# Optimization experiments

Measured on AMD Instinct MI355X. Metric: run time of the kernel, lower is better.

## Reference

```python
import jax, jax.numpy as jnp
import numpy as np

N_NODES = 50000
N_EDGES = 1600000
LORA_R = 8


def gcn_conv(h, W, b, src, dst, n):
    # PyG GCNConv: linear transform, add self-loops, symmetric normalization,
    # scatter-add aggregation at target nodes, then bias.
    h = h @ W  # [N, out]
    ones = jnp.ones(src.shape[0], dtype=h.dtype)
    deg = jax.ops.segment_sum(ones, dst, num_segments=n) + 1.0  # +1 for self-loop
    dis = jax.lax.rsqrt(deg)  # deg >= 1 always
    norm = dis[src] * dis[dst]  # [E]
    agg = jax.ops.segment_sum(norm[:, None] * h[src], dst, num_segments=n)
    agg = agg + (dis * dis)[:, None] * h  # self-loop contribution
    return agg + b


def lora(h, A, B):
    # LoRALinear: b(a(x)) * (1/r); replaces input (not additive)
    return (h @ A) @ B * (1.0 / LORA_R)


def setup_inputs() -> dict:
    key = jax.random.key(0)
    ks = jax.random.split(key, 12)
    inp = {}
    inp['x'] = jax.random.normal(ks[0], (N_NODES, 128), dtype=jnp.float32)
    inp['edge_index'] = jax.random.randint(ks[1], (2, N_EDGES), 0, N_NODES, dtype=jnp.int64 if jax.config.jax_enable_x64 else jnp.int32)
    inp['domain_idx'] = jax.random.randint(ks[2], (N_NODES,), 0, 3, dtype=jnp.int32)
    inp['emb_table'] = jax.random.normal(ks[3], (3, 4096), dtype=jnp.float32)
    s1 = 1.0 / np.sqrt(4224.0)
    inp['W1'] = jax.random.normal(ks[4], (4224, 32), dtype=jnp.float32) * s1
    inp['b1'] = jnp.zeros((32,), dtype=jnp.float32)
    inp['A1'] = jax.random.normal(ks[5], (32, LORA_R), dtype=jnp.float32) * (1.0 / np.sqrt(32.0))
    inp['B1'] = jax.random.normal(ks[6], (LORA_R, 32), dtype=jnp.float32) * (1.0 / np.sqrt(LORA_R))
    inp['W2'] = jax.random.normal(ks[7], (32, 5), dtype=jnp.float32) * (1.0 / np.sqrt(32.0))
    inp['b2'] = jnp.zeros((5,), dtype=jnp.float32)
    inp['A2'] = jax.random.normal(ks[8], (5, LORA_R), dtype=jnp.float32) * (1.0 / np.sqrt(5.0))
    inp['B2'] = jax.random.normal(ks[9], (LORA_R, 5), dtype=jnp.float32) * (1.0 / np.sqrt(LORA_R))
    return inp


def reference(x, edge_index, domain_idx, emb_table, W1, b1, A1, B1, W2, b2, A2, B2):
    n = x.shape[0]
    src, dst = edge_index[0], edge_index[1]
    embedded = emb_table[domain_idx]  # [N, 4096]
    h = jnp.concatenate([embedded, x], axis=1)  # [N, 4224]
    h = gcn_conv(h, W1, b1, src, dst, n)
    h = lora(h, A1, B1)
    h = jax.nn.relu(h)
    h = gcn_conv(h, W2, b2, src, dst, n)
    h = lora(h, A2, B2)
    return jax.nn.log_softmax(h, axis=1)
```

## Files before the change

kernel.cpp:

```cpp
#include <hip/hip_runtime.h>
#include <hip/hip_bf16.h>
#include <hip/hip_fp16.h>


#define XDIM 128
#define EMBDIM 4096
#define TB 4096
#define BSH 6
#define BN 64
#define ECAP2 2560

__global__ void __launch_bounds__(256) kA(
    const int* __restrict__ src, const int* __restrict__ dst,
    unsigned int* __restrict__ tedges, unsigned int* __restrict__ toffcnt,
    int e, int ntiles,
    const float* __restrict__ emb, const float* __restrict__ W1,
    float* __restrict__ emb_part,
    const float* __restrict__ A1, const float* __restrict__ A2,
    const float* __restrict__ B2, const float* __restrict__ b1,
    float* __restrict__ M2, float* __restrict__ b1A1,
    const float* __restrict__ x, float* __restrict__ g, int n) {
    __shared__ __align__(16) char smem[24576];
    int t = threadIdx.x, bx = blockIdx.x;
    if (bx < ntiles) {
        unsigned int* staged = (unsigned int*)smem;
        int* loff = (int*)(smem + 16384);
        int* rctr = (int*)(smem + 20480);
        int base = bx * TB;
        int len = min(TB, e - base);
        for (int i = t; i < 1024; i += 256) { loff[i] = 0; rctr[i] = 0; }
        __syncthreads();
        for (int i = t; i < len; i += 256) atomicAdd(&loff[dst[base + i] >> BSH], 1);
        __syncthreads();
        if (t < 64) {
            int ch = t * 16;
            int v[16]; int s0 = 0;
            #pragma unroll
            for (int k = 0; k < 16; ++k) { v[k] = loff[ch + k]; s0 += v[k]; }
            int pre = s0;
            #pragma unroll
            for (int d2 = 1; d2 < 64; d2 <<= 1) {
                int up = __shfl_up(pre, d2);
                if (t >= d2) pre += up;
            }
            int excl = pre - s0;
            unsigned int* ocp = toffcnt + (size_t)bx * 1024 + ch;
            #pragma unroll
            for (int k = 0; k < 16; ++k) {
                loff[ch + k] = excl;
                ocp[k] = ((unsigned int)excl << 16) | (unsigned int)v[k];
                excl += v[k];
            }
        }
        __syncthreads();
        for (int i = t; i < len; i += 256) {
            int s = src[base + i], d = dst[base + i];
            int b = d >> BSH;
            int r = atomicAdd(&rctr[b], 1);
            staged[loff[b] + r] = ((unsigned int)d << 16) | (unsigned int)s;
        }
        __syncthreads();
        uint4* tw = (uint4*)(tedges + (size_t)bx * TB);
        const uint4* sr = (const uint4*)staged;
        int lw = (len + 3) >> 2;
        for (int i = t; i < lw; i += 256) tw[i] = sr[i];
    } else if (bx < ntiles + 96) {
        float* red = (float*)smem;
        int bx2 = bx - ntiles;
        int dm = bx2 >> 5, seg = bx2 & 31;
        const float* er = emb + dm * EMBDIM + seg * 128;
        const float* wr = W1 + (size_t)(seg * 128) * 32;
        int j = t & 31, kk = t >> 5;
        float acc = 0.f;
        for (int k2 = kk; k2 < 128; k2 += 8) acc += er[k2] * wr[k2 * 32 + j];
        red[kk * 32 + j] = acc;
        __syncthreads();
        if (t < 32) {
            float s = 0.f;
            #pragma unroll
            for (int r = 0; r < 8; ++r) s += red[r * 32 + t];
            emb_part[bx2 * 32 + t] = s;
        }
        if (bx2 == 0) {
            if (t < 25) {
                int c = t / 5, cp = t % 5;
                float s = 0.f;
                #pragma unroll
                for (int r = 0; r < 8; ++r) s += A2[c * 8 + r] * B2[r * 5 + cp];
                M2[c * 5 + cp] = s * 0.125f;
            }
            if (t >= 32 && t < 40) {
                int j2 = t - 32;
                float s = 0.f;
                #pragma unroll
                for (int k = 0; k < 32; ++k) s += b1[k] * A1[k * 8 + j2];
                b1A1[j2] = s;
            }
        }
    } else {
        __half* xsh = (__half*)smem;
        float* sWA  = (float*)(smem + 16384);
        float* sA1  = (float*)(smem + 20480);
        int gb = bx - ntiles - 96;
        int row0 = gb * 64;
        sA1[t] = A1[t];
        for (int i = t; i < 2048; i += 256) {
            int row = i >> 5, c4 = i & 31;
            int gi = row0 + row;
            float4 v = (gi < n) ? ((const float4*)x)[(size_t)gi * 32 + c4]
                                : make_float4(0.f, 0.f, 0.f, 0.f);
            __half2 h01 = __floats2half2_rn(v.x, v.y);
            __half2 h23 = __floats2half2_rn(v.z, v.w);
            uint2 pk;
            pk.x = *(unsigned int*)&h01;
            pk.y = *(unsigned int*)&h23;
            *(uint2*)(xsh + row * 128 + c4 * 4) = pk;
        }
        __syncthreads();
        for (int idx = t; idx < 1024; idx += 256) {
            int k = idx >> 3, j = idx & 7;
            const float* wr = W1 + (size_t)(EMBDIM + k) * 32;
            float s = 0.f;
            #pragma unroll 8
            for (int c = 0; c < 32; ++c) s += wr[c] * sA1[c * 8 + j];
            sWA[idx] = s;
        }
        __syncthreads();
        int row = t >> 3, j = t & 7;
        const __half2* xr1 = (const __half2*)(xsh + row * 128);
        const __half2* xr2 = (const __half2*)(xsh + (row + 32) * 128);
        float acc1 = 0.f, acc2 = 0.f;
        #pragma unroll 8
        for (int k2 = 0; k2 < 64; ++k2) {
            float2 fa = __half22float2(xr1[k2]);
            float2 fb = __half22float2(xr2[k2]);
            float w0 = sWA[(2 * k2) * 8 + j];
            float w1 = sWA[(2 * k2 + 1) * 8 + j];
            acc1 += fa.x * w0 + fa.y * w1;
            acc2 += fb.x * w0 + fb.y * w1;
        }
        int gi1 = row0 + row, gi2 = row0 + row + 32;
        if (gi1 < n) g[(size_t)gi1 * 8 + j] = acc1;
        if (gi2 < n) g[(size_t)gi2 * 8 + j] = acc2;
    }
}

__global__ void __launch_bounds__(256) kB(
    const unsigned int* __restrict__ tedges, const unsigned int* __restrict__ toffcnt,
    int ntiles,
    const float* __restrict__ emb_part, const float* __restrict__ A1,
    const int* __restrict__ dom, const float* __restrict__ g,
    int* __restrict__ deg, __half* __restrict__ p1h,
    unsigned short* __restrict__ nsrc, unsigned int* __restrict__ bm, int n) {
    __shared__ int hist[64], eoff[64], rctr[64], sdom[64];
    __shared__ int mcur;
    __shared__ float sA1[256], sproj[96], sembA1[24];
    __shared__ __align__(16) unsigned int ebuf[ECAP2];
    __shared__ __align__(16) unsigned short esrc[ECAP2];
    int t = threadIdx.x, b = blockIdx.x;
    int row0 = b << BSH;
    if (t == 0) mcur = 0;
    if (t < 64) {
        hist[t] = 0; rctr[t] = 0;
        int gi = row0 + t;
        sdom[t] = (gi < n) ? dom[gi] : 0;
    }
    sA1[t] = A1[t];
    if (t < 96) {
        int dm = t >> 5, c = t & 31;
        float s = 0.f;
        #pragma unroll
        for (int seg = 0; seg < 32; ++seg) s += emb_part[(dm * 32 + seg) * 32 + c];
        sproj[dm * 32 + c] = s;
    }
    __syncthreads();
    for (int tl = t; tl < ntiles; tl += 256) {
        unsigned int oc = toffcnt[(size_t)tl * 1024 + b];
        int len = (int)(oc & 0xffffu);
        if (len > 0) {
            int dstb = atomicAdd(&mcur, len);
            const unsigned int* rp = tedges + (size_t)tl * TB + (oc >> 16);
            for (int j = 0; j < len; ++j) {
                int p = dstb + j;
                if (p < ECAP2) ebuf[p] = rp[j];
            }
        }
    }
    __syncthreads();
    int m = mcur;
    if (m > ECAP2) m = ECAP2;
    if (t == 0) bm[b] = (unsigned int)m;
    for (int i = t; i < m; i += 256) atomicAdd(&hist[(ebuf[i] >> 16) & (BN - 1)], 1);
    __syncthreads();
    if (t < 64) {
        int v = hist[t];
        int pre = v;
        #pragma unroll
        for (int d2 = 1; d2 < 64; d2 <<= 1) {
            int up = __shfl_up(pre, d2);
            if (t >= d2) pre += up;
        }
        eoff[t] = pre - v;
        int gi = row0 + t;
        if (gi < n) deg[gi] = v;
    } else if (t < 88) {
        int dm = (t - 64) >> 3, j = (t - 64) & 7;
        float s = 0.f;
        #pragma unroll 8
        for (int c = 0; c < 32; ++c) s += sproj[dm * 32 + c] * sA1[c * 8 + j];
        sembA1[dm * 8 + j] = s;
    }
    __syncthreads();
    for (int i = t; i < m; i += 256) {
        unsigned int u = ebuf[i];
        int dl = (int)(u >> 16) & (BN - 1);
        int r = atomicAdd(&rctr[dl], 1);
        esrc[eoff[dl] + r] = (unsigned short)(u & 0xffffu);
    }
    for (int i = t; i < 512; i += 256) {
        int row = i >> 3, j = i & 7;
        int gi = row0 + row;
        if (gi < n) {
            float dd = rsqrtf((float)(hist[row] + 1));
            float v = g[(size_t)gi * 8 + j] + sembA1[sdom[row] * 8 + j];
            p1h[(size_t)gi * 8 + j] = __float2half_rn(dd * v);
        }
    }
    __syncthreads();
    {
        uint4* npw = (uint4*)(nsrc + (size_t)b * ECAP2);
        const uint4* ew = (const uint4*)esrc;
        int mw = (m + 7) >> 3;
        for (int i = t; i < mw; i += 256) npw[i] = ew[i];
    }
}

__global__ void __launch_bounds__(256) k_bagg1(
    const __half* __restrict__ p1h, const unsigned short* __restrict__ nsrc,
    const unsigned int* __restrict__ bm, const int* __restrict__ deg,
    const float* __restrict__ b1A1, const float* __restrict__ B1,
    const float* __restrict__ W2, __half* __restrict__ qh, int n) {
    __shared__ __align__(16) unsigned short esrc[ECAP2];
    __shared__ int eoff[BN], sdeg[BN];
    __shared__ float pacc[3][BN][8];
    __shared__ float sB1[256], sW2[160], sb[8];
    int t = threadIdx.x, b = blockIdx.x;
    int node0 = b << BSH;
    sB1[t] = B1[t];
    if (t < 160) sW2[t] = W2[t];
    if (t < 8) sb[t] = b1A1[t];
    if (t < 64) {
        int node = node0 + t;
        int v = (node < n) ? deg[node] : 0;
        sdeg[t] = v;
        int pre = v;
        #pragma unroll
        for (int d2 = 1; d2 < 64; d2 <<= 1) {
            int up = __shfl_up(pre, d2);
            if (t >= d2) pre += up;
        }
        eoff[t] = pre - v;
    }
    __syncthreads();
    int m = (int)bm[b];
    if (m > ECAP2) m = ECAP2;
    {
        const uint4* npw = (const uint4*)(nsrc + (size_t)b * ECAP2);
        uint4* ew = (uint4*)esrc;
        int mw = (m + 7) >> 3;
        for (int i = t; i < mw; i += 256) ew[i] = npw[i];
    }
    __syncthreads();
    int nodeL = t & (BN - 1), tsub = t >> BSH;
    int base0 = eoff[nodeL], c = sdeg[nodeL];
    float a[8] = {0.f, 0.f, 0.f, 0.f, 0.f, 0.f, 0.f, 0.f};
    float a2[8] = {0.f, 0.f, 0.f, 0.f, 0.f, 0.f, 0.f, 0.f};
    int k = tsub;
    for (; k + 4 < c; k += 8) {
        int s1 = esrc[base0 + k], s2 = esrc[base0 + k + 4];
        uint4 u = *(const uint4*)(p1h + (size_t)s1 * 8);
        uint4 v = *(const uint4*)(p1h + (size_t)s2 * 8);
        float2 f;
        f = __half22float2(*(__half2*)&u.x); a[0] += f.x; a[1] += f.y;
        f = __half22float2(*(__half2*)&u.y); a[2] += f.x; a[3] += f.y;
        f = __half22float2(*(__half2*)&u.z); a[4] += f.x; a[5] += f.y;
        f = __half22float2(*(__half2*)&u.w); a[6] += f.x; a[7] += f.y;
        f = __half22float2(*(__half2*)&v.x); a2[0] += f.x; a2[1] += f.y;
        f = __half22float2(*(__half2*)&v.y); a2[2] += f.x; a2[3] += f.y;
        f = __half22float2(*(__half2*)&v.z); a2[4] += f.x; a2[5] += f.y;
        f = __half22float2(*(__half2*)&v.w); a2[6] += f.x; a2[7] += f.y;
    }
    for (; k < c; k += 4) {
        int s1 = esrc[base0 + k];
        uint4 u = *(const uint4*)(p1h + (size_t)s1 * 8);
        float2 f;
        f = __half22float2(*(__half2*)&u.x); a[0] += f.x; a[1] += f.y;
        f = __half22float2(*(__half2*)&u.y); a[2] += f.x; a[3] += f.y;
        f = __half22float2(*(__half2*)&u.z); a[4] += f.x; a[5] += f.y;
        f = __half22float2(*(__half2*)&u.w); a[6] += f.x; a[7] += f.y;
    }
    #pragma unroll
    for (int j = 0; j < 8; ++j) a[j] += a2[j];
    if (tsub > 0) {
        #pragma unroll
        for (int j = 0; j < 8; ++j) pacc[tsub - 1][nodeL][j] = a[j];
    }
    __syncthreads();
    if (t < BN) {
        int node = node0 + t;
        if (node < n) {
            float dd = rsqrtf((float)(sdeg[t] + 1));
            uint4 u = *(const uint4*)(p1h + (size_t)node * 8);
            float2 f;
            float af[8];
            f = __half22float2(*(__half2*)&u.x); af[0] = a[0] + f.x; af[1] = a[1] + f.y;
            f = __half22float2(*(__half2*)&u.y); af[2] = a[2] + f.x; af[3] = a[3] + f.y;
            f = __half22float2(*(__half2*)&u.z); af[4] = a[4] + f.x; af[5] = a[5] + f.y;
            f = __half22float2(*(__half2*)&u.w); af[6] = a[6] + f.x; af[7] = a[7] + f.y;
            #pragma unroll
            for (int ps = 0; ps < 3; ++ps) {
                #pragma unroll
                for (int j = 0; j < 8; ++j) af[j] += pacc[ps][t][j];
            }
            #pragma unroll
            for (int j = 0; j < 8; ++j) af[j] = dd * af[j] + sb[j];
            float qv[5] = {0.f, 0.f, 0.f, 0.f, 0.f};
            #pragma unroll
            for (int c2 = 0; c2 < 32; ++c2) {
                float tv = 0.f;
                #pragma unroll
                for (int j = 0; j < 8; ++j) tv += af[j] * sB1[j * 32 + c2];
                float st = fmaxf(tv * 0.125f, 0.f);
                #pragma unroll
                for (int o = 0; o < 5; ++o) qv[o] += st * sW2[c2 * 5 + o];
            }
            #pragma unroll
            for (int o = 0; o < 5; ++o) qh[(size_t)node * 8 + o] = __float2half_rn(dd * qv[o]);
        }
    }
}

__global__ void __launch_bounds__(256) k_bagg2(
    const __half* __restrict__ qh, const unsigned short* __restrict__ nsrc,
    const unsigned int* __restrict__ bm, const int* __restrict__ deg,
    const float* __restrict__ b2, const float* __restrict__ M2,
    float* __restrict__ out, int n) {
    __shared__ __align__(16) unsigned short esrc[ECAP2];
    __shared__ int eoff[BN], sdeg[BN];
    __shared__ float pacc[3][BN][5];
    __shared__ float sM2[25], sb2[5];
    int t = threadIdx.x, b = blockIdx.x;
    int node0 = b << BSH;
    if (t < 25) sM2[t] = M2[t];
    if (t < 5) sb2[t] = b2[t];
    if (t < 64) {
        int node = node0 + t;
        int v = (node < n) ? deg[node] : 0;
        sdeg[t] = v;
        int pre = v;
        #pragma unroll
        for (int d2 = 1; d2 < 64; d2 <<= 1) {
            int up = __shfl_up(pre, d2);
            if (t >= d2) pre += up;
        }
        eoff[t] = pre - v;
    }
    __syncthreads();
    int m = (int)bm[b];
    if (m > ECAP2) m = ECAP2;
    {
        const uint4* npw = (const uint4*)(nsrc + (size_t)b * ECAP2);
        uint4* ew = (uint4*)esrc;
        int mw = (m + 7) >> 3;
        for (int i = t; i < mw; i += 256) ew[i] = npw[i];
    }
    __syncthreads();
    int nodeL = t & (BN - 1), tsub = t >> BSH;
    int base0 = eoff[nodeL], c = sdeg[nodeL];
    float a[5] = {0.f, 0.f, 0.f, 0.f, 0.f};
    float a2[5] = {0.f, 0.f, 0.f, 0.f, 0.f};
    int k = tsub;
    for (; k + 4 < c; k += 8) {
        int s1 = esrc[base0 + k], s2 = esrc[base0 + k + 4];
        uint4 u = *(const uint4*)(qh + (size_t)s1 * 8);
        uint4 v = *(const uint4*)(qh + (size_t)s2 * 8);
        float2 f;
        f = __half22float2(*(__half2*)&u.x); a[0] += f.x; a[1] += f.y;
        f = __half22float2(*(__half2*)&u.y); a[2] += f.x; a[3] += f.y;
        f = __half22float2(*(__half2*)&u.z); a[4] += f.x;
        f = __half22float2(*(__half2*)&v.x); a2[0] += f.x; a2[1] += f.y;
        f = __half22float2(*(__half2*)&v.y); a2[2] += f.x; a2[3] += f.y;
        f = __half22float2(*(__half2*)&v.z); a2[4] += f.x;
    }
    for (; k < c; k += 4) {
        int s1 = esrc[base0 + k];
        uint4 u = *(const uint4*)(qh + (size_t)s1 * 8);
        float2 f;
        f = __half22float2(*(__half2*)&u.x); a[0] += f.x; a[1] += f.y;
        f = __half22float2(*(__half2*)&u.y); a[2] += f.x; a[3] += f.y;
        f = __half22float2(*(__half2*)&u.z); a[4] += f.x;
    }
    #pragma unroll
    for (int j = 0; j < 5; ++j) a[j] += a2[j];
    if (tsub > 0) {
        #pragma unroll
        for (int j = 0; j < 5; ++j) pacc[tsub - 1][nodeL][j] = a[j];
    }
    __syncthreads();
    if (t < BN) {
        int node = node0 + t;
        if (node < n) {
            float dd = rsqrtf((float)(sdeg[t] + 1));
            uint4 u = *(const uint4*)(qh + (size_t)node * 8);
            float2 f;
            float av[5];
            f = __half22float2(*(__half2*)&u.x); av[0] = a[0] + f.x; av[1] = a[1] + f.y;
            f = __half22float2(*(__half2*)&u.y); av[2] = a[2] + f.x; av[3] = a[3] + f.y;
            f = __half22float2(*(__half2*)&u.z); av[4] = a[4] + f.x;
            #pragma unroll
            for (int ps = 0; ps < 3; ++ps) {
                #pragma unroll
                for (int j = 0; j < 5; ++j) av[j] += pacc[ps][t][j];
            }
            #pragma unroll
            for (int j = 0; j < 5; ++j) av[j] = dd * av[j] + sb2[j];
            float z[5];
            #pragma unroll
            for (int cp = 0; cp < 5; ++cp) {
                float s = 0.f;
                #pragma unroll
                for (int c2 = 0; c2 < 5; ++c2) s += av[c2] * sM2[c2 * 5 + cp];
                z[cp] = s;
            }
            float mx = z[0];
            #pragma unroll
            for (int c2 = 1; c2 < 5; ++c2) mx = fmaxf(mx, z[c2]);
            float ssum = 0.f;
            #pragma unroll
            for (int c2 = 0; c2 < 5; ++c2) ssum += __expf(z[c2] - mx);
            float ls = __logf(ssum);
            #pragma unroll
            for (int c2 = 0; c2 < 5; ++c2) out[node * 5 + c2] = z[c2] - mx - ls;
        }
    }
}

extern "C" void kernel_launch(void* const* d_in, const int* in_sizes, int n_in,
                              void* d_out, int out_size, void* d_ws, size_t ws_size,
                              hipStream_t stream) {
    const float* x   = (const float*)d_in[0];
    const int*   ei  = (const int*)d_in[1];
    const int*   dom = (const int*)d_in[2];
    const float* emb = (const float*)d_in[3];
    const float* W1  = (const float*)d_in[4];
    const float* b1  = (const float*)d_in[5];
    const float* A1  = (const float*)d_in[6];
    const float* B1  = (const float*)d_in[7];
    const float* W2  = (const float*)d_in[8];
    const float* b2  = (const float*)d_in[9];
    const float* A2  = (const float*)d_in[10];
    const float* B2  = (const float*)d_in[11];
    float* out = (float*)d_out;

    int n = in_sizes[2];
    int e = in_sizes[1] / 2;
    const int* src = ei;
    const int* dst = ei + e;

    int ntiles = (e + TB - 1) / TB;
    int nbuck  = (n + BN - 1) >> BSH;
    int ngb    = (n + 63) / 64;

    char* base = (char*)d_ws;
    size_t o = 0;
    auto carve = [&](size_t bytes) {
        void* p = base + o;
        o = (o + bytes + 15) & ~(size_t)15;
        return p;
    };
    float* emb_part = (float*)carve(96 * 32 * sizeof(float));
    float* M2       = (float*)carve(32 * sizeof(float));
    float* b1A1     = (float*)carve(8 * sizeof(float));
    unsigned int* bm = (unsigned int*)carve(1024 * sizeof(int));
    int*   deg      = (int*)carve((size_t)n * sizeof(int));
    float* g        = (float*)carve((size_t)n * 8 * sizeof(float));
    __half* p1h     = (__half*)carve((size_t)n * 8 * sizeof(__half));
    __half* qh      = (__half*)carve((size_t)n * 8 * sizeof(__half));
    unsigned int* tedges  = (unsigned int*)carve((size_t)ntiles * TB * sizeof(unsigned int));
    unsigned int* toffcnt = (unsigned int*)carve((size_t)ntiles * 1024 * sizeof(unsigned int));
    unsigned short* nsrc  = (unsigned short*)carve((size_t)nbuck * ECAP2 * sizeof(unsigned short));
    (void)ws_size; (void)n_in; (void)out_size;

    kA<<<ntiles + 96 + ngb, 256, 0, stream>>>(
        src, dst, tedges, toffcnt, e, ntiles,
        emb, W1, emb_part, A1, A2, B2, b1, M2, b1A1, x, g, n);
    kB<<<nbuck, 256, 0, stream>>>(tedges, toffcnt, ntiles, emb_part, A1, dom, g,
                                  deg, p1h, nsrc, bm, n);
    k_bagg1<<<nbuck, 256, 0, stream>>>(p1h, nsrc, bm, deg, b1A1, B1, W2, qh, n);
    k_bagg2<<<nbuck, 256, 0, stream>>>(qh, nsrc, bm, deg, b2, M2, out, n);
}
```

Baseline: 158.0 us.

## Cache edge loads in registers and prefix-scan tile offsets for cooperative gather

```diff
diff --git a/kernel.cpp b/kernel.cpp
--- a/kernel.cpp
+++ b/kernel.cpp
@@ -9,6 +9,7 @@
 #define BSH 6
 #define BN 64
 #define ECAP2 2560
+#define MAXT 512
 
 __global__ void __launch_bounds__(256) kA(
     const int* __restrict__ src, const int* __restrict__ dst,
@@ -30,7 +31,20 @@
         int len = min(TB, e - base);
         for (int i = t; i < 1024; i += 256) { loff[i] = 0; rctr[i] = 0; }
         __syncthreads();
-        for (int i = t; i < len; i += 256) atomicAdd(&loff[dst[base + i] >> BSH], 1);
+        int sreg[16], dreg[16];
+        #pragma unroll
+        for (int k = 0; k < 16; ++k) {
+            int i = t + k * 256;
+            if (i < len) {
+                sreg[k] = src[base + i];
+                dreg[k] = dst[base + i];
+            }
+        }
+        #pragma unroll
+        for (int k = 0; k < 16; ++k) {
+            int i = t + k * 256;
+            if (i < len) atomicAdd(&loff[dreg[k] >> BSH], 1);
+        }
         __syncthreads();
         if (t < 64) {
             int ch = t * 16;
@@ -53,11 +67,14 @@
             }
         }
         __syncthreads();
-        for (int i = t; i < len; i += 256) {
-            int s = src[base + i], d = dst[base + i];
-            int b = d >> BSH;
-            int r = atomicAdd(&rctr[b], 1);
-            staged[loff[b] + r] = ((unsigned int)d << 16) | (unsigned int)s;
+        #pragma unroll
+        for (int k = 0; k < 16; ++k) {
+            int i = t + k * 256;
+            if (i < len) {
+                int b = dreg[k] >> BSH;
+                int r = atomicAdd(&rctr[b], 1);
+                staged[loff[b] + r] = ((unsigned int)dreg[k] << 16) | (unsigned int)sreg[k];
+            }
         }
         __syncthreads();
         uint4* tw = (uint4*)(tedges + (size_t)bx * TB);
@@ -153,13 +170,13 @@
     int* __restrict__ deg, __half* __restrict__ p1h,
     unsigned short* __restrict__ nsrc, unsigned int* __restrict__ bm, int n) {
     __shared__ int hist[64], eoff[64], rctr[64], sdom[64];
-    __shared__ int mcur;
+    __shared__ int mtot;
+    __shared__ unsigned short rbase[MAXT], soff[MAXT], slen[MAXT];
     __shared__ float sA1[256], sproj[96], sembA1[24];
     __shared__ __align__(16) unsigned int ebuf[ECAP2];
     __shared__ __align__(16) unsigned short esrc[ECAP2];
     int t = threadIdx.x, b = blockIdx.x;
     int row0 = b << BSH;
-    if (t == 0) mcur = 0;
     if (t < 64) {
         hist[t] = 0; rctr[t] = 0;
         int gi = row0 + t;
@@ -173,23 +190,47 @@
         for (int seg = 0; seg < 32; ++seg) s += emb_part[(dm * 32 + seg) * 32 + c];
         sproj[dm * 32 + c] = s;
     }
-    __syncthreads();
-    for (int tl = t; tl < ntiles; tl += 256) {
-        unsigned int oc = toffcnt[(size_t)tl * 1024 + b];
-        int len = (int)(oc & 0xffffu);
-        if (len > 0) {
-            int dstb = atomicAdd(&mcur, len);
-            const unsigned int* rp = tedges + (size_t)tl * TB + (oc >> 16);
-            for (int j = 0; j < len; ++j) {
-                int p = dstb + j;
-                if (p < ECAP2) ebuf[p] = rp[j];
-            }
-        }
-    }
-    __syncthreads();
-    int m = mcur;
+    if (t < 64) {
+        int carry = 0;
+        int nch = (ntiles + 63) >> 6;
+        for (int c = 0; c < nch; ++c) {
+            int idx = (c << 6) + t;
+            unsigned int oc = (idx < ntiles) ? toffcnt[(size_t)idx * 1024 + b] : 0u;
+            int l = (int)(oc & 0xffffu);
+            int pre = l;
+            #pragma unroll
+            for (int d2 = 1; d2 < 64; d2 <<= 1) {
+                int up = __shfl_up(pre, d2);
+                if (t >= d2) pre += up;
+            }
+            if (idx < ntiles) {
+                rbase[idx] = (unsigned short)min(carry + pre - l, 65535);
+                soff[idx]  = (unsigned short)(oc >> 16);
+                slen[idx]  = (unsigned short)l;
+            }
+            carry += __shfl(pre, 63);
+        }
+        if (t == 0) mtot = carry;
+    }
+    __syncthreads();
+    int m = mtot;
     if (m > ECAP2) m = ECAP2;
     if (t == 0) bm[b] = (unsigned int)m;
+    {
+        int g4 = t >> 2, l4 = t & 3;
+        for (int tl = g4; tl < ntiles; tl += 64) {
+            int l = slen[tl];
+            if (l > 0) {
+                const unsigned int* rp = tedges + (size_t)tl * TB + soff[tl];
+                int bse = rbase[tl];
+                for (int j = l4; j < l; j += 4) {
+                    int p = bse + j;
+                    if (p < ECAP2) ebuf[p] = rp[j];
+                }
+            }
+        }
+    }
+    __syncthreads();
     for (int i = t; i < m; i += 256) atomicAdd(&hist[(ebuf[i] >> 16) & (BN - 1)], 1);
     __syncthreads();
     if (t < 64) {
```

Measured after the change: 149.3 us. -5.5%, faster.
